# Kernel optimization log

Hardware: AMD Instinct MI355X
Metric: run time of the kernel (lower is better)

## Reference

```python
import jax, jax.numpy as jnp
import numpy as np

DIM = 96
EXPANSION = 2
INNER = DIM * EXPANSION        # 192
QKV_BLOCK = 4                  # per-head dim DH
NH = INNER // QKV_BLOCK        # 48 heads
CONV_K = 4
B, H, W = 2, 24, 24
EPS = 1e-5


def setup_inputs() -> dict:
    key = jax.random.key(0)
    ks = jax.random.split(key, 10)
    nrm = lambda k, shape, s=0.02: jax.random.normal(k, shape, dtype=jnp.float32) * s
    return {
        "x": jax.random.normal(ks[0], (B, DIM, H, W), dtype=jnp.float32),
        "ln_g": jnp.ones((DIM,), jnp.float32),
        "ln_b": jnp.zeros((DIM,), jnp.float32),
        "w_up": nrm(ks[1], (2 * INNER, DIM)),
        "b_up": jnp.zeros((2 * INNER,), jnp.float32),
        "w_q": nrm(ks[2], (NH, QKV_BLOCK, QKV_BLOCK), 0.2),
        "b_q": jnp.zeros((INNER,), jnp.float32),
        "w_k": nrm(ks[3], (NH, QKV_BLOCK, QKV_BLOCK), 0.2),
        "b_k": jnp.zeros((INNER,), jnp.float32),
        "w_v": nrm(ks[4], (NH, QKV_BLOCK, QKV_BLOCK), 0.2),
        "b_v": jnp.zeros((INNER,), jnp.float32),
        "w_conv": nrm(ks[5], (INNER, 1, CONV_K), 0.1),  # depthwise (O,I/g,K)
        "b_conv": jnp.zeros((INNER,), jnp.float32),
        "w_ig": nrm(ks[6], (NH, 3 * INNER)),
        "b_ig": jnp.zeros((NH,), jnp.float32),
        "w_fg": jnp.zeros((NH, 3 * INNER), jnp.float32),
        "b_fg": jnp.linspace(3.0, 6.0, NH, dtype=jnp.float32),  # xLSTM fgate bias init
        "on_g": jnp.ones((INNER,), jnp.float32),
        "on_b": jnp.zeros((INNER,), jnp.float32),
        "skip": jnp.ones((INNER,), jnp.float32),
        "w_down": nrm(ks[7], (DIM, INNER)),
        "b_down": jnp.zeros((DIM,), jnp.float32),
    }


def _layernorm(x, g, b):
    m = x.mean(-1, keepdims=True)
    v = x.var(-1, keepdims=True)
    return (x - m) / jnp.sqrt(v + EPS) * g + b


def _causal_conv(x, w, b):
    # x: (B,S,D); depthwise causal conv1d, left-pad K-1
    y = jax.lax.conv_general_dilated(
        x.transpose(0, 2, 1), w, (1,), [(CONV_K - 1, 0)],
        feature_group_count=INNER, dimension_numbers=("NCH", "OIH", "NCH"))
    return y.transpose(0, 2, 1) + b


def _headwise(x, w, b):
    # LinearHeadwiseExpand: block-diagonal per-head linear
    Bq, S, _ = x.shape
    xh = x.reshape(Bq, S, NH, QKV_BLOCK)
    return jnp.einsum("bsnd,nod->bsno", xh, w).reshape(Bq, S, INNER) + b


def _mlstm(q, k, v, ig, fg):
    # parallel_stabilized_simple; q,k,v: (B,NH,S,DH); ig,fg: (B,NH,S)
    S, DH = q.shape[2], q.shape[3]
    log_f = jax.nn.log_sigmoid(fg)                                           # (B,NH,S)
    lf_cum = jnp.concatenate(
        [jnp.zeros_like(log_f[..., :1]), jnp.cumsum(log_f, axis=-1)], axis=-1)  # (B,NH,S+1)
    log_fmat = lf_cum[..., :, None] - lf_cum[..., None, :]                   # (B,NH,S+1,S+1)
    ltr = jnp.tril(jnp.ones((S, S), dtype=bool))
    log_fg_mat = jnp.where(ltr, log_fmat[..., 1:, 1:], -jnp.inf)             # (B,NH,S,S)
    log_D = log_fg_mat + ig[..., None, :]
    max_log_D = jnp.max(log_D, axis=-1, keepdims=True)                       # rowwise stabilizer
    Dm = jnp.exp(log_D - max_log_D)
    qk = jnp.einsum("bhsd,bhtd->bhst", q, k) * (DH ** -0.5)
    Cm = qk * Dm
    normalizer = jnp.maximum(jnp.abs(Cm.sum(-1, keepdims=True)), jnp.exp(-max_log_D))
    return jnp.einsum("bhst,bhtd->bhsd", Cm / (normalizer + 1e-6), v)


def _mh_norm(h, g, b):
    # MultiHeadLayerNorm: per-head normalization over DH, then full affine
    m = h.mean(-1, keepdims=True)
    v = h.var(-1, keepdims=True)
    hn = (h - m) / jnp.sqrt(v + EPS)
    return hn * g.reshape(1, NH, 1, QKV_BLOCK) + b.reshape(1, NH, 1, QKV_BLOCK)


def reference(x, ln_g, ln_b, w_up, b_up, w_q, b_q, w_k, b_k, w_v, b_v,
              w_conv, b_conv, w_ig, b_ig, w_fg, b_fg, on_g, on_b, skip,
              w_down, b_down):
    Bb, C, Hh, Ww = x.shape
    S = Hh * Ww
    xs = x.reshape(Bb, C, S).transpose(0, 2, 1)                 # (B,S,C)
    h = _layernorm(xs, ln_g, ln_b)                              # ViLBlock pre-LN
    xi = h @ w_up.T + b_up                                      # (B,S,2*INNER)
    x_mlstm, z = jnp.split(xi, 2, axis=-1)
    x_conv = jax.nn.silu(_causal_conv(x_mlstm, w_conv, b_conv))
    q = _headwise(x_conv, w_q, b_q)
    k = _headwise(x_conv, w_k, b_k)
    v = _headwise(x_mlstm, w_v, b_v)
    qkv = jnp.concatenate([q, k, v], axis=-1)                   # (B,S,3*INNER)
    ig = jnp.einsum("bsf,hf->bhs", qkv, w_ig) + b_ig[None, :, None]
    fg = jnp.einsum("bsf,hf->bhs", qkv, w_fg) + b_fg[None, :, None]
    to_heads = lambda t: t.reshape(Bb, S, NH, QKV_BLOCK).transpose(0, 2, 1, 3)
    h_tilde = _mlstm(to_heads(q), to_heads(k), to_heads(v), ig, fg)   # (B,NH,S,DH)
    h_norm = _mh_norm(h_tilde, on_g, on_b).transpose(0, 2, 1, 3).reshape(Bb, S, INNER)
    h_skip = h_norm + skip * x_conv
    h_state = h_skip * jax.nn.silu(z)
    out = h_state @ w_down.T + b_down
    y = xs + out                                                # ViLBlock residual
    return y.transpose(0, 2, 1).reshape(Bb, C, Hh, Ww)
```

## Files before the change

kernel.cpp:

```cpp
#include <hip/hip_runtime.h>
#include <math.h>

#define SEQ   576
#define CDIM  96
#define INNER 192
#define NHEAD 48
#define DH    4
#define NB    2
#define EPSV  1e-5f
#define RT    64

__device__ __forceinline__ float silu_f(float x) { return x / (1.f + __expf(-x)); }
__device__ __forceinline__ float logsig_f(float x) {
    return (x >= 0.f) ? -log1pf(__expf(-x)) : (x - log1pf(__expf(x)));
}

__global__ void __launch_bounds__(512) k_ln_up(const float* __restrict__ x,
    const float* __restrict__ ln_g, const float* __restrict__ ln_b,
    const float* __restrict__ w_up, const float* __restrict__ b_up,
    float* __restrict__ xm, float* __restrict__ z) {
    const int t = threadIdx.x;
    const int p0 = blockIdx.x * 8;
    const int b = p0 / SEQ;
    const int f0 = blockIdx.y * 96;
    __shared__ __align__(16) float hbuf[8 * CDIM];

    {
        const int p = t >> 6, l = t & 63;
        const int s = (p0 + p) % SEQ;
        const float v0 = x[(size_t)(b * CDIM + l) * SEQ + s];
        const float v1 = (l < 32) ? x[(size_t)(b * CDIM + 64 + l) * SEQ + s] : 0.f;
        float sum = v0 + v1, sq = v0 * v0 + v1 * v1;
        #pragma unroll
        for (int off = 1; off < 64; off <<= 1) {
            sum += __shfl_xor(sum, off);
            sq  += __shfl_xor(sq, off);
        }
        const float mean = sum * (1.f / CDIM);
        const float rstd = rsqrtf(sq * (1.f / CDIM) - mean * mean + EPSV);
        hbuf[p * CDIM + l] = (v0 - mean) * rstd * ln_g[l] + ln_b[l];
        if (l < 32) hbuf[p * CDIM + 64 + l] = (v1 - mean) * rstd * ln_g[64 + l] + ln_b[64 + l];
    }
    __syncthreads();

    const int lane = t & 7, oi = t >> 3;
    const int p2 = oi & 7, fg = oi >> 3;
    const int pos = p0 + p2;
    const float4* hr = (const float4*)(hbuf + p2 * CDIM) + lane * 3;
    const float4 h0 = hr[0], h1 = hr[1], h2 = hr[2];
    #pragma unroll 4
    for (int j = 0; j < 12; ++j) {
        const int f = f0 + fg + 8 * j;
        const float4* wr = (const float4*)(w_up + (size_t)f * CDIM) + lane * 3;
        const float4 w0 = wr[0], w1 = wr[1], w2 = wr[2];
        float acc = h0.x*w0.x + h0.y*w0.y + h0.z*w0.z + h0.w*w0.w
                  + h1.x*w1.x + h1.y*w1.y + h1.z*w1.z + h1.w*w1.w
                  + h2.x*w2.x + h2.y*w2.y + h2.z*w2.z + h2.w*w2.w;
        #pragma unroll
        for (int off = 1; off < 8; off <<= 1) acc += __shfl_xor(acc, off);
        if (lane == 0) {
            acc += b_up[f];
            if (f < INNER) xm[(size_t)pos * INNER + f] = acc;
            else           z [(size_t)pos * INNER + (f - INNER)] = acc;
        }
    }
}

__global__ void __launch_bounds__(512) k_conv_qkv_gates(const float* __restrict__ xm,
    const float* __restrict__ w_conv, const float* __restrict__ b_conv,
    const float* __restrict__ w_q, const float* __restrict__ b_q,
    const float* __restrict__ w_k, const float* __restrict__ b_k,
    const float* __restrict__ w_v, const float* __restrict__ b_v,
    const float* __restrict__ w_ig, const float* __restrict__ b_ig,
    const float* __restrict__ w_fg, const float* __restrict__ b_fg,
    float* __restrict__ xc, float* __restrict__ qw, float* __restrict__ kw,
    float* __restrict__ vw, float* __restrict__ igw, float* __restrict__ fgw) {
    const int t = threadIdx.x;
    const int p0 = blockIdx.x * 4;
    const int b = p0 / SEQ, s0 = p0 % SEQ;
    __shared__ float xmb[7][INNER];
    __shared__ float xcb[4][INNER];
    __shared__ __align__(16) float qkvb[4][3 * INNER];

    for (int i = t; i < 7 * INNER; i += 512) {
        const int r = i / INNER, c = i % INNER;
        const int ss = s0 - 3 + r;
        xmb[r][c] = (ss >= 0) ? xm[(size_t)(b * SEQ + ss) * INNER + c] : 0.f;
    }
    __syncthreads();

    for (int i = t; i < 4 * INNER; i += 512) {
        const int p = i / INNER, c = i % INNER;
        float acc = b_conv[c];
        #pragma unroll
        for (int j = 0; j < 4; ++j) acc += xmb[p + j][c] * w_conv[c * 4 + j];
        const float v = silu_f(acc);
        xcb[p][c] = v;
        xc[(size_t)(b * SEQ + s0 + p) * INNER + c] = v;
    }
    __syncthreads();

    for (int i = t; i < 4 * INNER; i += 512) {
        const int p = i / INNER, c = i % INNER;
        const int n = c >> 2, o = c & 3;
        const float* wq = w_q + n * 16 + o * 4;
        const float* wk = w_k + n * 16 + o * 4;
        const float* wv = w_v + n * 16 + o * 4;
        float q = b_q[c], k = b_k[c], v = b_v[c];
        #pragma unroll
        for (int dd = 0; dd < 4; ++dd) {
            q += xcb[p][n * 4 + dd] * wq[dd];
            k += xcb[p][n * 4 + dd] * wk[dd];
            v += xmb[p + 3][n * 4 + dd] * wv[dd];
        }
        qkvb[p][c] = q; qkvb[p][INNER + c] = k; qkvb[p][2 * INNER + c] = v;
        const size_t base = ((size_t)(b * NHEAD + n) * SEQ + s0 + p) * DH + o;
        qw[base] = q; kw[base] = k; vw[base] = v;
    }
    __syncthreads();

    {
        const int w = t >> 6, l16 = t & 15, gg = (t >> 4) & 3;
        #pragma unroll
        for (int it = 0; it < 3; ++it) {
            const int g = w * 12 + it * 4 + gg;
            const bool isfg = (g >= NHEAD);
            const int hh = isfg ? (g - NHEAD) : g;
            const float4* wr = (const float4*)((isfg ? w_fg : w_ig) + (size_t)hh * 576) + l16 * 9;
            float4 wf[9];
            #pragma unroll
            for (int j = 0; j < 9; ++j) wf[j] = wr[j];
            #pragma unroll
            for (int p = 0; p < 4; ++p) {
                const float4* xr = (const float4*)(&qkvb[p][0]) + l16 * 9;
                float acc = 0.f;
                #pragma unroll
                for (int j = 0; j < 9; ++j) {
                    const float4 a = xr[j];
                    acc += a.x * wf[j].x + a.y * wf[j].y + a.z * wf[j].z + a.w * wf[j].w;
                }
                #pragma unroll
                for (int off = 1; off < 16; off <<= 1) acc += __shfl_xor(acc, off);
                if (l16 == 0) {
                    acc += isfg ? b_fg[hh] : b_ig[hh];
                    (isfg ? fgw : igw)[((size_t)b * NHEAD + hh) * SEQ + s0 + p] = acc;
                }
            }
        }
    }
}

__global__ void __launch_bounds__(512) k_mlstm(const float* __restrict__ qw,
    const float* __restrict__ kw, const float* __restrict__ vw,
    const float* __restrict__ igw, const float* __restrict__ fgw,
    float* __restrict__ ht) {
    const int bh = blockIdx.x;
    const int r0 = blockIdx.y * RT;
    const int nt = r0 + RT;
    const int t = threadIdx.x;
    __shared__ float4 k4[SEQ], v4[SEQ];
    __shared__ float m_l[SEQ], M_l[SEQ], lfc_l[SEQ];

    const float4* kb = (const float4*)(kw + (size_t)bh * SEQ * DH);
    const float4* vb = (const float4*)(vw + (size_t)bh * SEQ * DH);
    for (int i = t; i < nt; i += 512) { k4[i] = kb[i]; v4[i] = vb[i]; }

    if (t < 64) {
        const int base = t * 9;
        float pre[9], mv[9], mx[9];
        float run = 0.f;
        #pragma unroll
        for (int j = 0; j < 9; ++j) {
            run += logsig_f(fgw[(size_t)bh * SEQ + base + j]);
            pre[j] = run;
        }
        float incl = run;
        #pragma unroll
        for (int off = 1; off < 64; off <<= 1) {
            float o = __shfl_up(incl, off);
            if (t >= off) incl += o;
        }
        const float excl = incl - run;
        float runm = -INFINITY;
        #pragma unroll
        for (int j = 0; j < 9; ++j) {
            float lfc = excl + pre[j];
            lfc_l[base + j] = lfc;
            float mt = igw[(size_t)bh * SEQ + base + j] - lfc;
            mv[j] = mt;
            runm = fmaxf(runm, mt);
            mx[j] = runm;
        }
        float sc = runm;
        #pragma unroll
        for (int off = 1; off < 64; off <<= 1) {
            float o = __shfl_up(sc, off);
            if (t >= off) sc = fmaxf(sc, o);
        }
        float exclm = __shfl_up(sc, 1);
        if (t == 0) exclm = -INFINITY;
        #pragma unroll
        for (int j = 0; j < 9; ++j) {
            m_l[base + j] = mv[j];
            M_l[base + j] = fmaxf(exclm, mx[j]);
        }
    }
    __syncthreads();

    const int lane = t & 7;
    const int s0 = r0 + (t >> 3);
    const float4 q = ((const float4*)(qw + (size_t)bh * SEQ * DH))[s0];
    const float Ms = M_l[s0], lfcs = lfc_l[s0];

    float a0 = 0.f, a1 = 0.f, a2 = 0.f, a3 = 0.f, csum = 0.f;
    for (int tt = lane; tt <= s0; tt += 8) {
        const float e = __expf(m_l[tt] - Ms);
        const float4 kk = k4[tt], vv = v4[tt];
        const float c = (q.x*kk.x + q.y*kk.y + q.z*kk.z + q.w*kk.w) * 0.5f * e;
        csum += c;
        a0 += c * vv.x; a1 += c * vv.y; a2 += c * vv.z; a3 += c * vv.w;
    }
    #pragma unroll
    for (int off = 1; off < 8; off <<= 1) {
        csum += __shfl_xor(csum, off);
        a0 += __shfl_xor(a0, off); a1 += __shfl_xor(a1, off);
        a2 += __shfl_xor(a2, off); a3 += __shfl_xor(a3, off);
    }
    if (lane == 0) {
        const float floorv = __expf(-(lfcs + Ms));
        const float inv = 1.f / (fmaxf(fabsf(csum), floorv) + 1e-6f);
        ((float4*)ht)[(size_t)bh * SEQ + s0] =
            make_float4(a0 * inv, a1 * inv, a2 * inv, a3 * inv);
    }
}

__global__ void __launch_bounds__(256) k_epi(const float* __restrict__ ht,
    const float* __restrict__ on_g, const float* __restrict__ on_b,
    const float* __restrict__ skip, const float* __restrict__ xc,
    const float* __restrict__ zz, const float* __restrict__ w_down,
    const float* __restrict__ b_down, const float* __restrict__ x,
    float* __restrict__ out) {
    const int t = threadIdx.x;
    const int p0 = blockIdx.x * 2;
    const int b = p0 / SEQ;
    __shared__ __align__(16) float hs[2][INNER];

    for (int i = t; i < 2 * INNER; i += 256) {
        const int p = i / INNER, c = i % INNER;
        const int pos = p0 + p, s = pos % SEQ;
        const int n = c >> 2, o = c & 3;
        const float4 hv = ((const float4*)ht)[(size_t)(b * NHEAD + n) * SEQ + s];
        const float mean = (hv.x + hv.y + hv.z + hv.w) * 0.25f;
        const float d0 = hv.x - mean, d1 = hv.y - mean, d2 = hv.z - mean, d3 = hv.w - mean;
        const float var = (d0*d0 + d1*d1 + d2*d2 + d3*d3) * 0.25f;
        const float rstd = rsqrtf(var + EPSV);
        const float he = (o == 0) ? hv.x : (o == 1) ? hv.y : (o == 2) ? hv.z : hv.w;
        const float hn = (he - mean) * rstd * on_g[c] + on_b[c];
        const float hk = hn + skip[c] * xc[(size_t)pos * INNER + c];
        hs[p][c] = hk * silu_f(zz[(size_t)pos * INNER + c]);
    }
    __syncthreads();

    const int lane = t & 7, oi = t >> 3;
    const int p2 = oi & 1, cg2 = oi >> 1;
    const int pos = p0 + p2, s = pos % SEQ;
    const float4* hr = (const float4*)(&hs[p2][0]) + lane * 6;
    float4 h4[6];
    #pragma unroll
    for (int j = 0; j < 6; ++j) h4[j] = hr[j];
    #pragma unroll
    for (int j = 0; j < 6; ++j) {
        const int c = cg2 + 16 * j;
        const float4* wr = (const float4*)(w_down + (size_t)c * INNER) + lane * 6;
        float acc = 0.f;
        #pragma unroll
        for (int u = 0; u < 6; ++u) {
            const float4 w = wr[u];
            acc += h4[u].x*w.x + h4[u].y*w.y + h4[u].z*w.z + h4[u].w*w.w;
        }
        #pragma unroll
        for (int off = 1; off < 8; off <<= 1) acc += __shfl_xor(acc, off);
        if (lane == 0) {
            const size_t idx = ((size_t)b * CDIM + c) * SEQ + s;
            out[idx] = x[idx] + acc + b_down[c];
        }
    }
}

extern "C" void kernel_launch(void* const* d_in, const int* in_sizes, int n_in,
                              void* d_out, int out_size, void* d_ws, size_t ws_size,
                              hipStream_t stream) {
    const float* x      = (const float*)d_in[0];
    const float* ln_g   = (const float*)d_in[1];
    const float* ln_b   = (const float*)d_in[2];
    const float* w_up   = (const float*)d_in[3];
    const float* b_up   = (const float*)d_in[4];
    const float* w_q    = (const float*)d_in[5];
    const float* b_q    = (const float*)d_in[6];
    const float* w_k    = (const float*)d_in[7];
    const float* b_k    = (const float*)d_in[8];
    const float* w_v    = (const float*)d_in[9];
    const float* b_v    = (const float*)d_in[10];
    const float* w_conv = (const float*)d_in[11];
    const float* b_conv = (const float*)d_in[12];
    const float* w_ig   = (const float*)d_in[13];
    const float* b_ig   = (const float*)d_in[14];
    const float* w_fg   = (const float*)d_in[15];
    const float* b_fg   = (const float*)d_in[16];
    const float* on_g   = (const float*)d_in[17];
    const float* on_b   = (const float*)d_in[18];
    const float* skip   = (const float*)d_in[19];
    const float* w_down = (const float*)d_in[20];
    const float* b_down = (const float*)d_in[21];

    float* ws = (float*)d_ws;
    const size_t NSI = (size_t)NB * SEQ * INNER;
    const size_t NHS = (size_t)NB * NHEAD * SEQ;
    float* xm  = ws;
    float* z   = xm + NSI;
    float* xc  = z + NSI;
    float* qw  = xc + NSI;
    float* kw  = qw + NSI;
    float* vw  = kw + NSI;
    float* igw = vw + NSI;
    float* fgw = igw + NHS;
    float* ht  = fgw + NHS;

    float* out = (float*)d_out;

    hipLaunchKernelGGL(k_ln_up, dim3(NB * SEQ / 8, 4), dim3(512), 0, stream,
                       x, ln_g, ln_b, w_up, b_up, xm, z);
    hipLaunchKernelGGL(k_conv_qkv_gates, dim3(NB * SEQ / 4), dim3(512), 0, stream,
                       xm, w_conv, b_conv, w_q, b_q, w_k, b_k, w_v, b_v,
                       w_ig, b_ig, w_fg, b_fg, xc, qw, kw, vw, igw, fgw);
    hipLaunchKernelGGL(k_mlstm, dim3(NB * NHEAD, SEQ / RT), dim3(512), 0, stream,
                       qw, kw, vw, igw, fgw, ht);
    hipLaunchKernelGGL(k_epi, dim3(NB * SEQ / 2), dim3(256), 0, stream,
                       ht, on_g, on_b, skip, xc, z, w_down, b_down, x, out);
}
```

Baseline: 55.31 us.

## Shrink per-block work across all four kernels to launch more blocks

Each kernel now does less work per block so that more blocks are launched. The LN+up-projection handles 4 positions per block instead of 8, and the gate kernel splits the igate/fgate heads across a second grid dimension. The mLSTM row tile drops from 64 to 32 with 16 lanes per query row, and the epilogue handles one position per block. This targets low occupancy on the many compute units of an MI355X. The cost is redundant conv/qkv recomputation in the gate kernel's second y-slice, idle threads in LN and mLSTM, and more block launch overhead.

```diff
diff --git a/kernel.cpp b/kernel.cpp
--- a/kernel.cpp
+++ b/kernel.cpp
@@ -8,7 +8,7 @@
 #define DH    4
 #define NB    2
 #define EPSV  1e-5f
-#define RT    64
+#define RT    32
 
 __device__ __forceinline__ float silu_f(float x) { return x / (1.f + __expf(-x)); }
 __device__ __forceinline__ float logsig_f(float x) {
@@ -20,37 +20,39 @@
     const float* __restrict__ w_up, const float* __restrict__ b_up,
     float* __restrict__ xm, float* __restrict__ z) {
     const int t = threadIdx.x;
-    const int p0 = blockIdx.x * 8;
+    const int p0 = blockIdx.x * 4;
     const int b = p0 / SEQ;
     const int f0 = blockIdx.y * 96;
-    __shared__ __align__(16) float hbuf[8 * CDIM];
+    __shared__ __align__(16) float hbuf[4 * CDIM];
 
     {
         const int p = t >> 6, l = t & 63;
-        const int s = (p0 + p) % SEQ;
-        const float v0 = x[(size_t)(b * CDIM + l) * SEQ + s];
-        const float v1 = (l < 32) ? x[(size_t)(b * CDIM + 64 + l) * SEQ + s] : 0.f;
-        float sum = v0 + v1, sq = v0 * v0 + v1 * v1;
-        #pragma unroll
-        for (int off = 1; off < 64; off <<= 1) {
-            sum += __shfl_xor(sum, off);
-            sq  += __shfl_xor(sq, off);
-        }
-        const float mean = sum * (1.f / CDIM);
-        const float rstd = rsqrtf(sq * (1.f / CDIM) - mean * mean + EPSV);
-        hbuf[p * CDIM + l] = (v0 - mean) * rstd * ln_g[l] + ln_b[l];
-        if (l < 32) hbuf[p * CDIM + 64 + l] = (v1 - mean) * rstd * ln_g[64 + l] + ln_b[64 + l];
+        if (p < 4) {
+            const int s = (p0 + p) % SEQ;
+            const float v0 = x[(size_t)(b * CDIM + l) * SEQ + s];
+            const float v1 = (l < 32) ? x[(size_t)(b * CDIM + 64 + l) * SEQ + s] : 0.f;
+            float sum = v0 + v1, sq = v0 * v0 + v1 * v1;
+            #pragma unroll
+            for (int off = 1; off < 64; off <<= 1) {
+                sum += __shfl_xor(sum, off);
+                sq  += __shfl_xor(sq, off);
+            }
+            const float mean = sum * (1.f / CDIM);
+            const float rstd = rsqrtf(sq * (1.f / CDIM) - mean * mean + EPSV);
+            hbuf[p * CDIM + l] = (v0 - mean) * rstd * ln_g[l] + ln_b[l];
+            if (l < 32) hbuf[p * CDIM + 64 + l] = (v1 - mean) * rstd * ln_g[64 + l] + ln_b[64 + l];
+        }
     }
     __syncthreads();
 
     const int lane = t & 7, oi = t >> 3;
-    const int p2 = oi & 7, fg = oi >> 3;
+    const int p2 = oi & 3, fg = oi >> 2;
     const int pos = p0 + p2;
     const float4* hr = (const float4*)(hbuf + p2 * CDIM) + lane * 3;
     const float4 h0 = hr[0], h1 = hr[1], h2 = hr[2];
-    #pragma unroll 4
-    for (int j = 0; j < 12; ++j) {
-        const int f = f0 + fg + 8 * j;
+    #pragma unroll
+    for (int j = 0; j < 6; ++j) {
+        const int f = f0 + fg + 16 * j;
         const float4* wr = (const float4*)(w_up + (size_t)f * CDIM) + lane * 3;
         const float4 w0 = wr[0], w1 = wr[1], w2 = wr[2];
         float acc = h0.x*w0.x + h0.y*w0.y + h0.z*w0.z + h0.w*w0.w
@@ -77,6 +79,7 @@
     float* __restrict__ vw, float* __restrict__ igw, float* __restrict__ fgw) {
     const int t = threadIdx.x;
     const int p0 = blockIdx.x * 4;
+    const int y = blockIdx.y;
     const int b = p0 / SEQ, s0 = p0 % SEQ;
     __shared__ float xmb[7][INNER];
     __shared__ float xcb[4][INNER];
@@ -96,7 +99,7 @@
         for (int j = 0; j < 4; ++j) acc += xmb[p + j][c] * w_conv[c * 4 + j];
         const float v = silu_f(acc);
         xcb[p][c] = v;
-        xc[(size_t)(b * SEQ + s0 + p) * INNER + c] = v;
+        if (y == 0) xc[(size_t)(b * SEQ + s0 + p) * INNER + c] = v;
     }
     __syncthreads();
 
@@ -114,16 +117,20 @@
             v += xmb[p + 3][n * 4 + dd] * wv[dd];
         }
         qkvb[p][c] = q; qkvb[p][INNER + c] = k; qkvb[p][2 * INNER + c] = v;
-        const size_t base = ((size_t)(b * NHEAD + n) * SEQ + s0 + p) * DH + o;
-        qw[base] = q; kw[base] = k; vw[base] = v;
+        if (y == 0) {
+            const size_t base = ((size_t)(b * NHEAD + n) * SEQ + s0 + p) * DH + o;
+            qw[base] = q; kw[base] = k; vw[base] = v;
+        }
     }
     __syncthreads();
 
     {
         const int w = t >> 6, l16 = t & 15, gg = (t >> 4) & 3;
         #pragma unroll
-        for (int it = 0; it < 3; ++it) {
-            const int g = w * 12 + it * 4 + gg;
+        for (int it = 0; it < 2; ++it) {
+            const int sub = it * 4 + gg;
+            if (sub >= 6) break;
+            const int g = y * 48 + w * 6 + sub;
             const bool isfg = (g >= NHEAD);
             const int hh = isfg ? (g - NHEAD) : g;
             const float4* wr = (const float4*)((isfg ? w_fg : w_ig) + (size_t)hh * 576) + l16 * 9;
@@ -207,13 +214,13 @@
     }
     __syncthreads();
 
-    const int lane = t & 7;
-    const int s0 = r0 + (t >> 3);
+    const int lane = t & 15;
+    const int s0 = r0 + (t >> 4);
     const float4 q = ((const float4*)(qw + (size_t)bh * SEQ * DH))[s0];
     const float Ms = M_l[s0], lfcs = lfc_l[s0];
 
     float a0 = 0.f, a1 = 0.f, a2 = 0.f, a3 = 0.f, csum = 0.f;
-    for (int tt = lane; tt <= s0; tt += 8) {
+    for (int tt = lane; tt <= s0; tt += 16) {
         const float e = __expf(m_l[tt] - Ms);
         const float4 kk = k4[tt], vv = v4[tt];
         const float c = (q.x*kk.x + q.y*kk.y + q.z*kk.z + q.w*kk.w) * 0.5f * e;
@@ -221,7 +228,7 @@
         a0 += c * vv.x; a1 += c * vv.y; a2 += c * vv.z; a3 += c * vv.w;
     }
     #pragma unroll
-    for (int off = 1; off < 8; off <<= 1) {
+    for (int off = 1; off < 16; off <<= 1) {
         csum += __shfl_xor(csum, off);
         a0 += __shfl_xor(a0, off); a1 += __shfl_xor(a1, off);
         a2 += __shfl_xor(a2, off); a3 += __shfl_xor(a3, off);
@@ -241,13 +248,12 @@
     const float* __restrict__ b_down, const float* __restrict__ x,
     float* __restrict__ out) {
     const int t = threadIdx.x;
-    const int p0 = blockIdx.x * 2;
-    const int b = p0 / SEQ;
-    __shared__ __align__(16) float hs[2][INNER];
-
-    for (int i = t; i < 2 * INNER; i += 256) {
-        const int p = i / INNER, c = i % INNER;
-        const int pos = p0 + p, s = pos % SEQ;
+    const int pos = blockIdx.x;
+    const int b = pos / SEQ, s = pos % SEQ;
+    __shared__ __align__(16) float hs[INNER];
+
+    if (t < INNER) {
+        const int c = t;
         const int n = c >> 2, o = c & 3;
         const float4 hv = ((const float4*)ht)[(size_t)(b * NHEAD + n) * SEQ + s];
         const float mean = (hv.x + hv.y + hv.z + hv.w) * 0.25f;
@@ -257,20 +263,18 @@
         const float he = (o == 0) ? hv.x : (o == 1) ? hv.y : (o == 2) ? hv.z : hv.w;
         const float hn = (he - mean) * rstd * on_g[c] + on_b[c];
         const float hk = hn + skip[c] * xc[(size_t)pos * INNER + c];
-        hs[p][c] = hk * silu_f(zz[(size_t)pos * INNER + c]);
-    }
-    __syncthreads();
-
-    const int lane = t & 7, oi = t >> 3;
-    const int p2 = oi & 1, cg2 = oi >> 1;
-    const int pos = p0 + p2, s = pos % SEQ;
-    const float4* hr = (const float4*)(&hs[p2][0]) + lane * 6;
+        hs[c] = hk * silu_f(zz[(size_t)pos * INNER + c]);
+    }
+    __syncthreads();
+
+    const int lane = t & 7, cg2 = t >> 3;
+    const float4* hr = (const float4*)hs + lane * 6;
     float4 h4[6];
     #pragma unroll
     for (int j = 0; j < 6; ++j) h4[j] = hr[j];
     #pragma unroll
-    for (int j = 0; j < 6; ++j) {
-        const int c = cg2 + 16 * j;
+    for (int j = 0; j < 3; ++j) {
+        const int c = cg2 + 32 * j;
         const float4* wr = (const float4*)(w_down + (size_t)c * INNER) + lane * 6;
         float acc = 0.f;
         #pragma unroll
@@ -328,13 +332,13 @@
 
     float* out = (float*)d_out;
 
-    hipLaunchKernelGGL(k_ln_up, dim3(NB * SEQ / 8, 4), dim3(512), 0, stream,
+    hipLaunchKernelGGL(k_ln_up, dim3(NB * SEQ / 4, 4), dim3(512), 0, stream,
                        x, ln_g, ln_b, w_up, b_up, xm, z);
-    hipLaunchKernelGGL(k_conv_qkv_gates, dim3(NB * SEQ / 4), dim3(512), 0, stream,
+    hipLaunchKernelGGL(k_conv_qkv_gates, dim3(NB * SEQ / 4, 2), dim3(512), 0, stream,
                        xm, w_conv, b_conv, w_q, b_q, w_k, b_k, w_v, b_v,
                        w_ig, b_ig, w_fg, b_fg, xc, qw, kw, vw, igw, fgw);
     hipLaunchKernelGGL(k_mlstm, dim3(NB * NHEAD, SEQ / RT), dim3(512), 0, stream,
                        qw, kw, vw, igw, fgw, ht);
-    hipLaunchKernelGGL(k_epi, dim3(NB * SEQ / 2), dim3(256), 0, stream,
+    hipLaunchKernelGGL(k_epi, dim3(NB * SEQ), dim3(256), 0, stream,
                        ht, on_g, on_b, skip, xc, z, w_down, b_down, x, out);
 }
```

Result: slower. 57.84 us (+4.6%).
